# Kernel optimization log

Measured on AMD Instinct MI355X. Metric: run time of the kernel, lower is better.

## Reference

```python
import jax, jax.numpy as jnp
import numpy as np

B, S, V, E, HD, T = 64, 512, 32000, 256, 1024, 9
H = HD // 2  # per-direction hidden


def _lstm_dir(x, w_ih, w_hh, b_ih, b_hh, reverse):
    # x: [B,S,I]; w_ih: [4H,I]; w_hh: [4H,H]  (PyTorch gate order i,f,g,o)
    xg = jnp.einsum('bsi,gi->bsg', x, w_ih) + b_ih + b_hh  # [B,S,4H]
    nb = x.shape[0]
    hdim = w_hh.shape[1]

    def step(carry, xg_t):
        h, c = carry
        g = xg_t + h @ w_hh.T
        i, f, gg, o = jnp.split(g, 4, axis=-1)
        c = jax.nn.sigmoid(f) * c + jax.nn.sigmoid(i) * jnp.tanh(gg)
        h = jax.nn.sigmoid(o) * jnp.tanh(c)
        return (h, c), h

    init = (jnp.zeros((nb, hdim), x.dtype), jnp.zeros((nb, hdim), x.dtype))
    _, hs = jax.lax.scan(step, init, jnp.swapaxes(xg, 0, 1), reverse=reverse)
    return jnp.swapaxes(hs, 0, 1)  # [B,S,H]


def _bilstm_layer(x, w_ih, w_hh, b_ih, b_hh):
    fwd = _lstm_dir(x, w_ih[0], w_hh[0], b_ih[0], b_hh[0], False)
    bwd = _lstm_dir(x, w_ih[1], w_hh[1], b_ih[1], b_hh[1], True)
    return jnp.concatenate([fwd, bwd], axis=-1)


def _crf_loss(emissions, labels, mask, trans, start_t, end_t, valid_lens):
    # emissions [B,S,T], labels [B,S] int, mask [B,S] bool
    maskf = mask.astype(emissions.dtype)
    em = jnp.take_along_axis(emissions, labels[..., None], -1)[..., 0]  # [B,S]
    tr = trans[labels[:, :-1], labels[:, 1:]]  # [B,S-1]
    last_tag = jnp.take_along_axis(labels, (valid_lens - 1)[:, None], 1)[:, 0]
    num = (start_t[labels[:, 0]] + em[:, 0]
           + ((em[:, 1:] + tr) * maskf[:, 1:]).sum(-1)
           + end_t[last_tag])

    alpha0 = start_t[None, :] + emissions[:, 0]  # [B,T]

    def step(alpha, inp):
        em_t, m_t = inp  # [B,T], [B]
        nxt = jax.nn.logsumexp(alpha[:, :, None] + trans[None], axis=1) + em_t
        return jnp.where(m_t[:, None], nxt, alpha), None

    alpha, _ = jax.lax.scan(step, alpha0,
                            (jnp.swapaxes(emissions[:, 1:], 0, 1),
                             jnp.swapaxes(mask[:, 1:], 0, 1)))
    logZ = jax.nn.logsumexp(alpha + end_t[None, :], axis=-1)
    llh = num - logZ
    return -jnp.mean(llh)  # reduction='mean' over batch, negated in forward


def _crf_decode(emissions, mask, trans, start_t, end_t):
    score0 = start_t[None, :] + emissions[:, 0]  # [B,T]

    def step(score, inp):
        em_t, m_t = inp
        cand = score[:, :, None] + trans[None]  # [B,T(prev),T(cur)]
        best_prev = jnp.argmax(cand, axis=1)  # [B,T]
        new = jnp.max(cand, axis=1) + em_t
        score = jnp.where(m_t[:, None], new, score)
        return score, best_prev

    score, hist = jax.lax.scan(step, score0,
                               (jnp.swapaxes(emissions[:, 1:], 0, 1),
                                jnp.swapaxes(mask[:, 1:], 0, 1)))
    best_last = jnp.argmax(score + end_t[None, :], axis=-1)  # [B]

    def bt(tag, inp):
        hist_t, m_t = inp  # [B,T], [B]
        prev = jnp.take_along_axis(hist_t, tag[:, None], 1)[:, 0]
        tag = jnp.where(m_t, prev, tag)
        return tag, tag

    _, ys = jax.lax.scan(bt, best_last,
                         (hist, jnp.swapaxes(mask[:, 1:], 0, 1)),
                         reverse=True)  # [S-1,B]
    tags = jnp.concatenate([ys, best_last[None]], axis=0)  # [S,B]
    return jnp.swapaxes(tags, 0, 1)  # [B,S]


def setup_inputs() -> dict:
    key = jax.random.key(0)
    ks = jax.random.split(key, 16)
    sc = 0.05
    inp = {
        'input_ids': jax.random.randint(ks[0], (B, S), 0, V, dtype=jnp.int32),
        'valid_lens': jax.random.randint(ks[1], (B,), 1, S + 1, dtype=jnp.int32),
        'labels': jax.random.randint(ks[2], (B, S), 0, T, dtype=jnp.int32),
        'emb': jax.random.normal(ks[3], (V, E), jnp.float32) * sc,
        'w_ih0': jax.random.normal(ks[4], (2, 4 * H, E), jnp.float32) * sc,
        'w_hh0': jax.random.normal(ks[5], (2, 4 * H, H), jnp.float32) * sc,
        'b_ih0': jax.random.normal(ks[6], (2, 4 * H), jnp.float32) * sc,
        'b_hh0': jax.random.normal(ks[7], (2, 4 * H), jnp.float32) * sc,
        'w_ih1': jax.random.normal(ks[8], (2, 4 * H, HD), jnp.float32) * sc,
        'w_hh1': jax.random.normal(ks[9], (2, 4 * H, H), jnp.float32) * sc,
        'b_ih1': jax.random.normal(ks[10], (2, 4 * H), jnp.float32) * sc,
        'b_hh1': jax.random.normal(ks[11], (2, 4 * H), jnp.float32) * sc,
        'cls_w': jax.random.normal(ks[12], (T, HD), jnp.float32) * sc,
        'cls_b': jax.random.normal(ks[13], (T,), jnp.float32) * sc,
        'trans': jax.random.normal(ks[14], (T, T), jnp.float32) * sc,
        'start_t': jax.random.normal(ks[15], (T,), jnp.float32) * sc,
    }
    inp['end_t'] = jax.random.normal(jax.random.fold_in(key, 99), (T,), jnp.float32) * sc
    return inp


def reference(input_ids, valid_lens, labels, emb, w_ih0, w_hh0, b_ih0, b_hh0,
              w_ih1, w_hh1, b_ih1, b_hh1, cls_w, cls_b, trans, start_t, end_t):
    x = emb[input_ids]  # [B,S,E]
    x = _bilstm_layer(x, w_ih0, w_hh0, b_ih0, b_hh0)   # [B,S,HD]
    x = _bilstm_layer(x, w_ih1, w_hh1, b_ih1, b_hh1)   # [B,S,HD]
    # dropout is identity in eval mode
    logits = jnp.einsum('bsh,th->bst', x, cls_w) + cls_b  # [B,S,T]
    mask = jnp.arange(input_ids.shape[1])[None, :] < valid_lens[:, None]
    tag_ids = _crf_decode(logits, mask, trans, start_t, end_t)
    loss = _crf_loss(logits, labels, mask, trans, start_t, end_t, valid_lens)
    return tag_ids, loss
```

## Files before the change

kernel.cpp:

```cpp
#include <hip/hip_runtime.h>
#include <hip/hip_fp8.h>
#include <math.h>

#define BB 64
#define SS 512
#define EE 256
#define HH 512
#define HD 1024
#define TT 9
#define MM (BB*SS)

typedef __attribute__((ext_vector_type(8))) short    short8;
typedef __attribute__((ext_vector_type(4))) float    f32x4;
typedef __attribute__((ext_vector_type(4))) unsigned uint4v;

__device__ __forceinline__ unsigned short f2bfu(float x) {
    unsigned b = __float_as_uint(x);
    b += 0x7FFFu + ((b >> 16) & 1u);
    return (unsigned short)(b >> 16);
}
__device__ __forceinline__ unsigned pack2bf(float lo, float hi) {
    return ((unsigned)f2bfu(hi) << 16) | (unsigned)f2bfu(lo);
}

__global__ void zero_kernel(float* __restrict__ p, int n)
{
    int i = blockIdx.x * blockDim.x + threadIdx.x;
    int stride = gridDim.x * blockDim.x;
    for (; i < n; i += stride) p[i] = 0.f;
}

__global__ void pack_kernel(const float* __restrict__ w_ih, const float* __restrict__ w_hh,
                            unsigned short* __restrict__ dst, int KX, int nf, int total)
{
    int tid = blockIdx.x * 256 + threadIdx.x;
    if (tid >= total) return;
    int j    = tid & 7;
    int lane = (tid >> 3) & 63;
    int f    = (tid >> 9) % nf;
    int rest = (tid >> 9) / nf;
    int jb   = rest & 127;
    int d    = rest >> 7;
    int m = lane & 15, quad = lane >> 4;
    int jj = m >> 2, q = m & 3;
    int row = q * HH + jb * 4 + jj;
    int k   = f * 32 + quad * 8 + j;
    float v;
    if (k < KX) v = w_ih[((size_t)d * 2048 + row) * (size_t)KX + k];
    else        v = w_hh[((size_t)d * 2048 + row) * (size_t)HH + (k - KX)];
    dst[tid] = f2bfu(v);
}

template<int LAYER>
__global__ __launch_bounds__(256, 1)
void bilstm_persist(const int* __restrict__ ids, const float* __restrict__ emb,
                    const unsigned short* __restrict__ x1,
                    const unsigned short* __restrict__ packA,
                    const float* __restrict__ b_ih, const float* __restrict__ b_hh,
                    unsigned short* hbuf,
                    unsigned short* __restrict__ h0out,
                    unsigned char*  __restrict__ h1out,
                    unsigned* cnt)
{
    constexpr int KX = LAYER ? HD : EE;
    constexpr int NF = (KX + HH) / 32;
    constexpr int XF = KX / 32;
    constexpr int HF = HH / 32;
    constexpr int XG = XF / 8;

    const int bid  = blockIdx.x;
    const int d    = bid >> 7;
    const int jb   = bid & 127;
    const int tid  = threadIdx.x;
    const int lane = tid & 63;
    const int wv   = tid >> 6;
    const int quad = lane >> 4;
    const int ln15 = lane & 15;
    const int b    = wv * 16 + ln15;
    const int u    = jb * 4 + quad;

    const uint4v* myA = (const uint4v*)(packA + (size_t)(d * 128 + jb) * NF * 512);
    uint4v Ar[NF];
    #pragma unroll
    for (int f = 0; f < NF; f++) Ar[f] = myA[f * 64 + lane];

    float bias_[4];
    #pragma unroll
    for (int q = 0; q < 4; q++)
        bias_[q] = b_ih[d * 2048 + q * HH + u] + b_hh[d * 2048 + q * HH + u];

    unsigned* myc = cnt + d * 16;
    float c_ = 0.f;

    for (int s = 0; s < SS; s++) {
        const int t = d ? (SS - 1 - s) : s;
        const int p = s & 1;
        f32x4 acc = {0.f, 0.f, 0.f, 0.f};

        const float*          erow = nullptr;
        const unsigned short* xrow = nullptr;
        if (LAYER == 0) erow = emb + (size_t)ids[b * SS + t] * EE;
        else            xrow = x1 + ((size_t)(b * SS + t)) * HD;

        auto loadBx = [&](int f) -> uint4v {
            const int k0 = f * 32 + quad * 8;
            if (LAYER == 0) {
                float4 f0 = *(const float4*)(erow + k0);
                float4 f1 = *(const float4*)(erow + k0 + 4);
                uint4v r;
                r[0] = pack2bf(f0.x, f0.y); r[1] = pack2bf(f0.z, f0.w);
                r[2] = pack2bf(f1.x, f1.y); r[3] = pack2bf(f1.z, f1.w);
                return r;
            } else {
                return *(const uint4v*)(xrow + k0);
            }
        };

        uint4v Bg[2][8];
        #pragma unroll
        for (int jx = 0; jx < 8; jx++) Bg[0][jx] = loadBx(jx);
        #pragma unroll
        for (int g = 0; g < XG; g++) {
            const int cur = g & 1;
            if (g + 1 < XG) {
                #pragma unroll
                for (int jx = 0; jx < 8; jx++)
                    Bg[cur ^ 1][jx] = loadBx((g + 1) * 8 + jx);
            }
            #pragma unroll
            for (int jx = 0; jx < 8; jx++) {
                short8 a  = __builtin_bit_cast(short8, Ar[g * 8 + jx]);
                short8 bv = __builtin_bit_cast(short8, Bg[cur][jx]);
                acc = __builtin_amdgcn_mfma_f32_16x16x32_bf16(a, bv, acc, 0, 0, 0);
            }
        }

        if (tid == 0) {
            const unsigned tgt = 128u * (unsigned)s;
            while (__hip_atomic_load(myc, __ATOMIC_RELAXED,
                                     __HIP_MEMORY_SCOPE_AGENT) < tgt)
                __builtin_amdgcn_s_sleep(2);
        }
        __atomic_signal_fence(__ATOMIC_ACQ_REL);
        __syncthreads();

        {
            const unsigned long long* hp = (const unsigned long long*)
                (hbuf + ((size_t)((d * 2 + p) * BB + b)) * HH);
            uint4v Bh[HF];
            #pragma unroll
            for (int f = 0; f < HF; f++) {
                unsigned long long l0 = __hip_atomic_load(hp + f * 8 + quad * 2,
                                          __ATOMIC_RELAXED, __HIP_MEMORY_SCOPE_AGENT);
                unsigned long long l1 = __hip_atomic_load(hp + f * 8 + quad * 2 + 1,
                                          __ATOMIC_RELAXED, __HIP_MEMORY_SCOPE_AGENT);
                uint4v r;
                r[0] = (unsigned)l0; r[1] = (unsigned)(l0 >> 32);
                r[2] = (unsigned)l1; r[3] = (unsigned)(l1 >> 32);
                Bh[f] = r;
            }
            #pragma unroll
            for (int f = 0; f < HF; f++) {
                short8 a  = __builtin_bit_cast(short8, Ar[XF + f]);
                short8 bv = __builtin_bit_cast(short8, Bh[f]);
                acc = __builtin_amdgcn_mfma_f32_16x16x32_bf16(a, bv, acc, 0, 0, 0);
            }
        }

        float gi = acc[0] + bias_[0];
        float gf = acc[1] + bias_[1];
        float gg = acc[2] + bias_[2];
        float go = acc[3] + bias_[3];
        float i_ = 1.f / (1.f + __expf(-gi));
        float f_ = 1.f / (1.f + __expf(-gf));
        float xg = fminf(fmaxf(gg, -15.f), 15.f);
        float e2 = __expf(2.f * xg);
        float g_ = (e2 - 1.f) / (e2 + 1.f);
        float o_ = 1.f / (1.f + __expf(-go));
        c_ = f_ * c_ + i_ * g_;
        float xc  = fminf(fmaxf(c_, -15.f), 15.f);
        float e2c = __expf(2.f * xc);
        float hn  = o_ * ((e2c - 1.f) / (e2c + 1.f));

        int hb = (int)f2bfu(hn);
        int ob = __shfl_xor(hb, 16);
        if (!(quad & 1)) {
            unsigned v32 = (unsigned)(unsigned short)hb
                         | ((unsigned)(unsigned short)ob << 16);
            __hip_atomic_store((unsigned*)(hbuf +
                ((size_t)((d * 2 + (p ^ 1)) * BB + b)) * HH + u),
                v32, __ATOMIC_RELAXED, __HIP_MEMORY_SCOPE_AGENT);
            if (LAYER == 0)
                *(unsigned*)(h0out + ((size_t)(b * SS + t)) * HD + d * HH + u) = v32;
        }
        if (LAYER == 1) {
            __hip_fp8_e4m3 f8(hn);
            int b8  = (int)f8.__x;
            int o8  = __shfl_xor(b8, 16);
            int pr  = (b8 & 0xff) | ((o8 & 0xff) << 8);
            int pr2 = __shfl_xor(pr, 32);
            if (quad == 0) {
                unsigned val = (unsigned)(pr & 0xffff) | ((unsigned)(pr2 & 0xffff) << 16);
                *(unsigned*)(h1out + ((size_t)(b * SS + t)) * HD + d * HH + jb * 4) = val;
            }
        }

        __syncthreads();
        __atomic_signal_fence(__ATOMIC_ACQ_REL);
        if (tid == 0)
            __hip_atomic_fetch_add(myc, 1u, __ATOMIC_RELAXED, __HIP_MEMORY_SCOPE_AGENT);
    }
}

__global__ __launch_bounds__(256)
void logits_fp8(const unsigned char* __restrict__ h1, const float* __restrict__ cls_w,
                float* __restrict__ out)
{
    __shared__ float Wc[TT * HD];
    const int tid = threadIdx.x;
    for (int i = tid; i < TT * HD; i += 256) Wc[i] = cls_w[i];
    __syncthreads();
    const int lane = tid & 63;
    const int row  = blockIdx.x * 4 + (tid >> 6);
    const unsigned char* xr = h1 + (size_t)row * HD;
    float p[TT] = {};
    #pragma unroll
    for (int it = 0; it < 16; it++) {
        __hip_fp8_e4m3 f8; f8.__x = xr[it * 64 + lane];
        float xv = (float)f8;
        #pragma unroll
        for (int n = 0; n < TT; n++) p[n] += xv * Wc[n * HD + it * 64 + lane];
    }
    #pragma unroll
    for (int n = 0; n < TT; n++) {
        float v = p[n];
        #pragma unroll
        for (int off = 32; off > 0; off >>= 1) v += __shfl_down(v, off);
        if (lane == 0) out[(size_t)row * TT + n] = v;
    }
}

__global__ __launch_bounds__(64)
void crf_kernel(const float* __restrict__ logits, const int* __restrict__ labels,
                const int* __restrict__ vlens, const float* __restrict__ trans,
                const float* __restrict__ start_t, const float* __restrict__ end_t,
                const float* __restrict__ cls_b,
                float* __restrict__ tags_out, float* __restrict__ llh)
{
    const int b = blockIdx.x;
    const int lane = threadIdx.x;
    const int len = vlens[b];
    const float* em = logits + (size_t)b * (SS * TT);
    const int*  lab = labels + (size_t)b * SS;
    __shared__ unsigned char hist[(SS - 1) * TT];

    float cb = (lane < TT) ? cls_b[lane] : 0.f;
    float tcol[TT];
    #pragma unroll
    for (int i = 0; i < TT; i++) tcol[i] = (lane < TT) ? trans[i * TT + lane] : 0.f;
    float score = (lane < TT) ? (start_t[lane] + em[lane] + cb) : 0.f;
    float alpha = score;
    float num = 0.f; int plab = 0;
    if (lane == 0) { plab = lab[0]; num = start_t[plab] + em[plab] + cls_b[plab]; }

    for (int t = 1; t < SS; t++) {
        float emj = (lane < TT) ? (em[t * TT + lane] + cb) : 0.f;
        float sv[TT], av[TT];
        #pragma unroll
        for (int i = 0; i < TT; i++) { sv[i] = __shfl(score, i); av[i] = __shfl(alpha, i); }
        float best = -INFINITY; int bp = 0; float amx = -INFINITY;
        #pragma unroll
        for (int i = 0; i < TT; i++) {
            float cnd = sv[i] + tcol[i];
            if (cnd > best) { best = cnd; bp = i; }
            amx = fmaxf(amx, av[i] + tcol[i]);
        }
        float se = 0.f;
        #pragma unroll
        for (int i = 0; i < TT; i++) se += expf(av[i] + tcol[i] - amx);
        const bool m = (t < len);
        if (m) { score = best + emj; alpha = amx + logf(se) + emj; }
        if (lane < TT) hist[(t - 1) * TT + lane] = (unsigned char)bp;
        if (lane == 0 && m) {
            int lt = lab[t];
            num += em[t * TT + lt] + cls_b[lt] + trans[plab * TT + lt];
            plab = lt;
        }
    }
    float fsc[TT], fal[TT];
    #pragma unroll
    for (int i = 0; i < TT; i++) { fsc[i] = __shfl(score, i); fal[i] = __shfl(alpha, i); }
    __syncthreads();
    if (lane == 0) {
        num += end_t[lab[len - 1]];
        int bl = 0; float bv = fsc[0] + end_t[0];
        #pragma unroll
        for (int i = 1; i < TT; i++) {
            float v = fsc[i] + end_t[i];
            if (v > bv) { bv = v; bl = i; }
        }
        float zmx = -INFINITY;
        #pragma unroll
        for (int i = 0; i < TT; i++) zmx = fmaxf(zmx, fal[i] + end_t[i]);
        float zse = 0.f;
        #pragma unroll
        for (int i = 0; i < TT; i++) zse += expf(fal[i] + end_t[i] - zmx);
        llh[b] = num - (zmx + logf(zse));
        int tag = bl;
        tags_out[b * SS + (SS - 1)] = (float)tag;
        for (int t = SS - 2; t >= 0; t--) {
            if (t + 1 < len) tag = hist[t * TT + tag];
            tags_out[b * SS + t] = (float)tag;
        }
    }
}

__global__ void loss_kernel(const float* __restrict__ llh, float* __restrict__ out)
{
    float v = llh[threadIdx.x];
    #pragma unroll
    for (int off = 32; off > 0; off >>= 1) v += __shfl_down(v, off);
    if (threadIdx.x == 0) out[MM] = -(v / 64.f);
}

extern "C" void kernel_launch(void* const* d_in, const int* in_sizes, int n_in,
                              void* d_out, int out_size, void* d_ws, size_t ws_size,
                              hipStream_t stream)
{
    const int*   ids     = (const int*)  d_in[0];
    const int*   vlen    = (const int*)  d_in[1];
    const int*   labels  = (const int*)  d_in[2];
    const float* emb     = (const float*)d_in[3];
    const float* w_ih0   = (const float*)d_in[4];
    const float* w_hh0   = (const float*)d_in[5];
    const float* b_ih0   = (const float*)d_in[6];
    const float* b_hh0   = (const float*)d_in[7];
    const float* w_ih1   = (const float*)d_in[8];
    const float* w_hh1   = (const float*)d_in[9];
    const float* b_ih1   = (const float*)d_in[10];
    const float* b_hh1   = (const float*)d_in[11];
    const float* cls_w   = (const float*)d_in[12];
    const float* cls_b   = (const float*)d_in[13];
    const float* trans   = (const float*)d_in[14];
    const float* start_t = (const float*)d_in[15];
    const float* end_t   = (const float*)d_in[16];

    float*          llh    = (float*)d_ws;
    unsigned*       cnt    = (unsigned*)(llh + 64);
    unsigned short* hbuf0  = (unsigned short*)(cnt + 64);
    unsigned short* hbuf1  = hbuf0 + 131072;
    unsigned short* h0out  = hbuf1 + 131072;
    unsigned short* packA1 = h0out + (size_t)MM * HD;
    float*          logits = (float*)packA1;
    unsigned short* packA0 = packA1 + 6291456;
    unsigned char*  h1out  = (unsigned char*)packA0;

    zero_kernel<<<512, 256, 0, stream>>>((float*)cnt, 64 + (131072 + 131072) / 2);

    pack_kernel<<<(3145728 + 255) / 256, 256, 0, stream>>>(w_ih0, w_hh0, packA0, EE, 24, 3145728);
    pack_kernel<<<(6291456 + 255) / 256, 256, 0, stream>>>(w_ih1, w_hh1, packA1, HD, 48, 6291456);

    bilstm_persist<0><<<256, 256, 0, stream>>>(
        ids, emb, nullptr, packA0, b_ih0, b_hh0, hbuf0, h0out, nullptr, cnt);
    bilstm_persist<1><<<256, 256, 0, stream>>>(
        ids, nullptr, h0out, packA1, b_ih1, b_hh1, hbuf1, nullptr, h1out, cnt + 32);

    logits_fp8<<<MM / 4, 256, 0, stream>>>(h1out, cls_w, logits);
    crf_kernel<<<BB, 64, 0, stream>>>(logits, labels, vlen, trans, start_t, end_t,
                                      cls_b, (float*)d_out, llh);
    loss_kernel<<<1, 64, 0, stream>>>(llh, (float*)d_out);
}
```

Measured before the change: 10.52 ms.

## Replace per-direction block counter with per-wave batch-group flags in persistent BiLSTM

Remaps the persistent LSTM blocks so each block handles one 16-row batch group and each wave owns a distinct hidden-unit slice. The single per-direction atomic counter and its block-wide barriers are replaced by per-wave step flags that waves poll directly. Each wave now waits only on the 128 producers of its own batch group rather than on every block in the direction. All input-projection loads are issued before the wait, and layer 0 caches token ids in shared memory. This trades larger register pressure from the fully unrolled input loads, plus more flag polling traffic, for less global synchronisation latency on the recurrent critical path.

```diff
diff --git a/kernel.cpp b/kernel.cpp
--- a/kernel.cpp
+++ b/kernel.cpp
@@ -60,24 +60,37 @@
                     unsigned short* hbuf,
                     unsigned short* __restrict__ h0out,
                     unsigned char*  __restrict__ h1out,
-                    unsigned* cnt)
+                    unsigned* flags)
 {
     constexpr int KX = LAYER ? HD : EE;
     constexpr int NF = (KX + HH) / 32;
     constexpr int XF = KX / 32;
     constexpr int HF = HH / 32;
-    constexpr int XG = XF / 8;
+    constexpr int XFA = (LAYER == 0) ? XF : 1;
+    constexpr int XFB = (LAYER == 1) ? XF : 1;
+
+    __shared__ int sid[16 * 513];
 
     const int bid  = blockIdx.x;
     const int d    = bid >> 7;
-    const int jb   = bid & 127;
+    const int g    = (bid >> 5) & 3;
+    const int ub   = bid & 31;
     const int tid  = threadIdx.x;
     const int lane = tid & 63;
     const int wv   = tid >> 6;
     const int quad = lane >> 4;
     const int ln15 = lane & 15;
-    const int b    = wv * 16 + ln15;
+    const int b    = g * 16 + ln15;
+    const int jb   = ub * 4 + wv;
     const int u    = jb * 4 + quad;
+
+    if (LAYER == 0) {
+        for (int i = tid; i < 16 * 512; i += 256) {
+            int r = i >> 9, cc = i & 511;
+            sid[r * 513 + cc] = ids[(g * 16 + r) * SS + cc];
+        }
+        __syncthreads();
+    }
 
     const uint4v* myA = (const uint4v*)(packA + (size_t)(d * 128 + jb) * NF * 512);
     uint4v Ar[NF];
@@ -89,7 +102,9 @@
     for (int q = 0; q < 4; q++)
         bias_[q] = b_ih[d * 2048 + q * HH + u] + b_hh[d * 2048 + q * HH + u];
 
-    unsigned* myc = cnt + d * 16;
+    unsigned* gflags = flags + (d * 4 + g) * 128;
+    const unsigned long long* fq = (const unsigned long long*)gflags;
+
     float c_ = 0.f;
 
     for (int s = 0; s < SS; s++) {
@@ -97,74 +112,73 @@
         const int p = s & 1;
         f32x4 acc = {0.f, 0.f, 0.f, 0.f};
 
-        const float*          erow = nullptr;
-        const unsigned short* xrow = nullptr;
-        if (LAYER == 0) erow = emb + (size_t)ids[b * SS + t] * EE;
-        else            xrow = x1 + ((size_t)(b * SS + t)) * HD;
-
-        auto loadBx = [&](int f) -> uint4v {
-            const int k0 = f * 32 + quad * 8;
-            if (LAYER == 0) {
-                float4 f0 = *(const float4*)(erow + k0);
-                float4 f1 = *(const float4*)(erow + k0 + 4);
+        float4 Fa[XFA], Fb[XFA];
+        uint4v Bx[XFB];
+        if constexpr (LAYER == 0) {
+            const float* erow = emb + (size_t)sid[ln15 * 513 + t] * EE;
+            #pragma unroll
+            for (int f = 0; f < XF; f++) {
+                const int k0 = f * 32 + quad * 8;
+                Fa[f] = *(const float4*)(erow + k0);
+                Fb[f] = *(const float4*)(erow + k0 + 4);
+            }
+        } else {
+            const unsigned short* xrow = x1 + ((size_t)(b * SS + t)) * HD;
+            #pragma unroll
+            for (int f = 0; f < XF; f++)
+                Bx[f] = *(const uint4v*)(xrow + f * 32 + quad * 8);
+        }
+        __builtin_amdgcn_sched_barrier(0);
+
+        if (s) {
+            const unsigned tgt = (unsigned)s;
+            while (1) {
+                unsigned long long q = __hip_atomic_load(fq + lane,
+                                         __ATOMIC_RELAXED, __HIP_MEMORY_SCOPE_AGENT);
+                if (__all(((unsigned)q >= tgt) & ((unsigned)(q >> 32) >= tgt))) break;
+                __builtin_amdgcn_s_sleep(1);
+            }
+            __atomic_signal_fence(__ATOMIC_ACQ_REL);
+        }
+
+        const unsigned long long* hp = (const unsigned long long*)
+            (hbuf + ((size_t)((d * 2 + p) * BB + b)) * HH);
+        unsigned long long hl0[HF], hl1[HF];
+        #pragma unroll
+        for (int f = 0; f < HF; f++) {
+            hl0[f] = __hip_atomic_load(hp + f * 8 + quad * 2,
+                        __ATOMIC_RELAXED, __HIP_MEMORY_SCOPE_AGENT);
+            hl1[f] = __hip_atomic_load(hp + f * 8 + quad * 2 + 1,
+                        __ATOMIC_RELAXED, __HIP_MEMORY_SCOPE_AGENT);
+        }
+        __builtin_amdgcn_sched_barrier(0);
+
+        if constexpr (LAYER == 0) {
+            #pragma unroll
+            for (int f = 0; f < XF; f++) {
                 uint4v r;
-                r[0] = pack2bf(f0.x, f0.y); r[1] = pack2bf(f0.z, f0.w);
-                r[2] = pack2bf(f1.x, f1.y); r[3] = pack2bf(f1.z, f1.w);
-                return r;
-            } else {
-                return *(const uint4v*)(xrow + k0);
+                r[0] = pack2bf(Fa[f].x, Fa[f].y); r[1] = pack2bf(Fa[f].z, Fa[f].w);
+                r[2] = pack2bf(Fb[f].x, Fb[f].y); r[3] = pack2bf(Fb[f].z, Fb[f].w);
+                acc = __builtin_amdgcn_mfma_f32_16x16x32_bf16(
+                        __builtin_bit_cast(short8, Ar[f]),
+                        __builtin_bit_cast(short8, r), acc, 0, 0, 0);
             }
-        };
-
-        uint4v Bg[2][8];
-        #pragma unroll
-        for (int jx = 0; jx < 8; jx++) Bg[0][jx] = loadBx(jx);
-        #pragma unroll
-        for (int g = 0; g < XG; g++) {
-            const int cur = g & 1;
-            if (g + 1 < XG) {
-                #pragma unroll
-                for (int jx = 0; jx < 8; jx++)
-                    Bg[cur ^ 1][jx] = loadBx((g + 1) * 8 + jx);
-            }
+        } else {
             #pragma unroll
-            for (int jx = 0; jx < 8; jx++) {
-                short8 a  = __builtin_bit_cast(short8, Ar[g * 8 + jx]);
-                short8 bv = __builtin_bit_cast(short8, Bg[cur][jx]);
-                acc = __builtin_amdgcn_mfma_f32_16x16x32_bf16(a, bv, acc, 0, 0, 0);
-            }
-        }
-
-        if (tid == 0) {
-            const unsigned tgt = 128u * (unsigned)s;
-            while (__hip_atomic_load(myc, __ATOMIC_RELAXED,
-                                     __HIP_MEMORY_SCOPE_AGENT) < tgt)
-                __builtin_amdgcn_s_sleep(2);
-        }
-        __atomic_signal_fence(__ATOMIC_ACQ_REL);
-        __syncthreads();
-
-        {
-            const unsigned long long* hp = (const unsigned long long*)
-                (hbuf + ((size_t)((d * 2 + p) * BB + b)) * HH);
-            uint4v Bh[HF];
-            #pragma unroll
-            for (int f = 0; f < HF; f++) {
-                unsigned long long l0 = __hip_atomic_load(hp + f * 8 + quad * 2,
-                                          __ATOMIC_RELAXED, __HIP_MEMORY_SCOPE_AGENT);
-                unsigned long long l1 = __hip_atomic_load(hp + f * 8 + quad * 2 + 1,
-                                          __ATOMIC_RELAXED, __HIP_MEMORY_SCOPE_AGENT);
-                uint4v r;
-                r[0] = (unsigned)l0; r[1] = (unsigned)(l0 >> 32);
-                r[2] = (unsigned)l1; r[3] = (unsigned)(l1 >> 32);
-                Bh[f] = r;
-            }
-            #pragma unroll
-            for (int f = 0; f < HF; f++) {
-                short8 a  = __builtin_bit_cast(short8, Ar[XF + f]);
-                short8 bv = __builtin_bit_cast(short8, Bh[f]);
-                acc = __builtin_amdgcn_mfma_f32_16x16x32_bf16(a, bv, acc, 0, 0, 0);
-            }
+            for (int f = 0; f < XF; f++)
+                acc = __builtin_amdgcn_mfma_f32_16x16x32_bf16(
+                        __builtin_bit_cast(short8, Ar[f]),
+                        __builtin_bit_cast(short8, Bx[f]), acc, 0, 0, 0);
+        }
+
+        #pragma unroll
+        for (int f = 0; f < HF; f++) {
+            uint4v r;
+            r[0] = (unsigned)hl0[f]; r[1] = (unsigned)(hl0[f] >> 32);
+            r[2] = (unsigned)hl1[f]; r[3] = (unsigned)(hl1[f] >> 32);
+            acc = __builtin_amdgcn_mfma_f32_16x16x32_bf16(
+                    __builtin_bit_cast(short8, Ar[XF + f]),
+                    __builtin_bit_cast(short8, r), acc, 0, 0, 0);
         }
 
         float gi = acc[0] + bias_[0];
@@ -205,10 +219,10 @@
             }
         }
 
-        __syncthreads();
-        __atomic_signal_fence(__ATOMIC_ACQ_REL);
-        if (tid == 0)
-            __hip_atomic_fetch_add(myc, 1u, __ATOMIC_RELAXED, __HIP_MEMORY_SCOPE_AGENT);
+        asm volatile("s_waitcnt vmcnt(0)" ::: "memory");
+        if (lane == 0)
+            __hip_atomic_store(gflags + jb, (unsigned)(s + 1),
+                               __ATOMIC_RELAXED, __HIP_MEMORY_SCOPE_AGENT);
     }
 }
 
@@ -346,8 +360,8 @@
     const float* end_t   = (const float*)d_in[16];
 
     float*          llh    = (float*)d_ws;
-    unsigned*       cnt    = (unsigned*)(llh + 64);
-    unsigned short* hbuf0  = (unsigned short*)(cnt + 64);
+    unsigned*       flags  = (unsigned*)(llh + 64);
+    unsigned short* hbuf0  = (unsigned short*)(flags + 2048);
     unsigned short* hbuf1  = hbuf0 + 131072;
     unsigned short* h0out  = hbuf1 + 131072;
     unsigned short* packA1 = h0out + (size_t)MM * HD;
@@ -355,15 +369,15 @@
     unsigned short* packA0 = packA1 + 6291456;
     unsigned char*  h1out  = (unsigned char*)packA0;
 
-    zero_kernel<<<512, 256, 0, stream>>>((float*)cnt, 64 + (131072 + 131072) / 2);
+    zero_kernel<<<512, 256, 0, stream>>>((float*)flags, 2048 + (131072 + 131072) / 2);
 
     pack_kernel<<<(3145728 + 255) / 256, 256, 0, stream>>>(w_ih0, w_hh0, packA0, EE, 24, 3145728);
     pack_kernel<<<(6291456 + 255) / 256, 256, 0, stream>>>(w_ih1, w_hh1, packA1, HD, 48, 6291456);
 
     bilstm_persist<0><<<256, 256, 0, stream>>>(
-        ids, emb, nullptr, packA0, b_ih0, b_hh0, hbuf0, h0out, nullptr, cnt);
+        ids, emb, nullptr, packA0, b_ih0, b_hh0, hbuf0, h0out, nullptr, flags);
     bilstm_persist<1><<<256, 256, 0, stream>>>(
-        ids, nullptr, h0out, packA1, b_ih1, b_hh1, hbuf1, nullptr, h1out, cnt + 32);
+        ids, nullptr, h0out, packA1, b_ih1, b_hh1, hbuf1, nullptr, h1out, flags + 1024);
 
     logits_fp8<<<MM / 4, 256, 0, stream>>>(h1out, cls_w, logits);
     crf_kernel<<<BB, 64, 0, stream>>>(logits, labels, vlen, trans, start_t, end_t,
```

After: 8.433 ms. 1.25x faster.
